# Kernel optimization log

Hardware: AMD Instinct MI355X
Metric: run time of the kernel (lower is better)

Reference implementation:

```python
import jax, jax.numpy as jnp
import numpy as np


def conv2d(x, w, b, pad):
    y = jax.lax.conv_general_dilated(x, w, (1, 1), [(pad, pad), (pad, pad)],
                                     dimension_numbers=('NCHW', 'OIHW', 'NCHW'))
    return y + b[None, :, None, None]


def setup_inputs() -> dict:
    key = jax.random.key(0)
    ks = jax.random.split(key, 24)
    bs, C, OC, K = 2, 64, 3, 3
    hi = wi = 96
    ho = wo = 192

    def _w(k, o, i, kh, kw):
        return jax.random.normal(k, (o, i, kh, kw), jnp.float32) / np.float32(np.sqrt(i * kh * kw))

    inp = {
        'x': jax.random.normal(ks[0], (bs, C, hi, wi), jnp.float32),
        'poseMap': jax.random.normal(ks[1], (1, 3, ho, wo), jnp.float32),
        'interMapY': jax.random.randint(ks[2], (ho, wo), 0, hi, jnp.int32),
        'interMapX': jax.random.randint(ks[3], (ho, wo), 0, wi, jnp.int32),
        # sigmaconv: 3x3 convs 64->64->64->2
        'sig_w1': _w(ks[4], 64, 64, 3, 3), 'sig_b1': jnp.zeros((64,), jnp.float32),
        'sig_w2': _w(ks[5], 64, 64, 3, 3), 'sig_b2': jnp.zeros((64,), jnp.float32),
        'sig_w3': _w(ks[6], 2, 64, 3, 3), 'sig_b3': jnp.zeros((2,), jnp.float32),
        # dwconv: 1x1 convs 3->64->256->C*K*K
        'dw_w1': _w(ks[7], 64, 3, 1, 1), 'dw_b1': jnp.zeros((64,), jnp.float32),
        'dw_w2': _w(ks[8], 256, 64, 1, 1), 'dw_b2': jnp.zeros((256,), jnp.float32),
        'dw_w3': _w(ks[9], C * K * K, 256, 1, 1), 'dw_b3': jnp.zeros((C * K * K,), jnp.float32),
        # pwconv: 1x1 convs 3->64->256->C*OC
        'pw_w1': _w(ks[10], 64, 3, 1, 1), 'pw_b1': jnp.zeros((64,), jnp.float32),
        'pw_w2': _w(ks[11], 256, 64, 1, 1), 'pw_b2': jnp.zeros((256,), jnp.float32),
        'pw_w3': _w(ks[12], C * OC, 256, 1, 1), 'pw_b3': jnp.zeros((C * OC,), jnp.float32),
    }
    return inp


def reference(x, poseMap, interMapY, interMapX,
              sig_w1, sig_b1, sig_w2, sig_b2, sig_w3, sig_b3,
              dw_w1, dw_b1, dw_w2, dw_b2, dw_w3, dw_b3,
              pw_w1, pw_b1, pw_w2, pw_b2, pw_w3, pw_b3):
    C, K, OC = 64, 3, 3
    bs, _, hi, wi = x.shape
    ho, wo = poseMap.shape[2], poseMap.shape[3]
    pad = K // 2

    p = jax.lax.stop_gradient(poseMap)  # original detaches poseMap
    # kernel-predict branches (1x1 conv MLPs over position map)
    dw = conv2d(jax.nn.relu(conv2d(jax.nn.relu(conv2d(p, dw_w1, dw_b1, 0)), dw_w2, dw_b2, 0)), dw_w3, dw_b3, 0)
    dw = dw.reshape(1, C, K * K, ho, wo)
    pw = conv2d(jax.nn.relu(conv2d(jax.nn.relu(conv2d(p, pw_w1, pw_b1, 0)), pw_w2, pw_b2, 0)), pw_w3, pw_b3, 0)
    pw = pw.reshape(C, OC, ho, wo)

    # unfold(x, K, padding=K//2): [bs, C, K*K, hi, wi], kernel taps row-major
    xp = jnp.pad(x, ((0, 0), (0, 0), (pad, pad), (pad, pad)))
    h = jnp.stack([xp[:, :, dy:dy + hi, dx:dx + wi]
                   for dy in range(K) for dx in range(K)], axis=2)
    # irregular spatial gather to HR grid: [bs, C, K*K, ho, wo]
    h = h[:, :, :, interMapY, interMapX]

    mean = jnp.sum(h * jax.nn.softmax(dw, axis=2), axis=2)  # [bs, C, ho, wo]
    sigma = conv2d(jax.nn.relu(conv2d(jax.nn.relu(conv2d(mean, sig_w1, sig_b1, 1)), sig_w2, sig_b2, 1)), sig_w3, sig_b3, 1)
    sigmad = sigma[:, 0:1, None, :, :]
    sigmar = sigma[:, 1:2, None, :, :]
    bw = sigmad * dw + sigmar * jnp.abs(h - mean[:, :, None, :, :])
    xa = jnp.sum(h * jax.nn.softmax(bw, axis=2), axis=2)  # [bs, C, ho, wo]
    out = jnp.einsum('bchw,cohw->bohw', xa, pw)  # [bs, OC, ho, wo]
    return out
```

## Files before the change

kernel.cpp:

```cpp
#include <hip/hip_runtime.h>
#include <hip/hip_bf16.h>

#define NPIX 36864

typedef __attribute__((ext_vector_type(8))) short short8;
typedef __attribute__((ext_vector_type(4))) short short4v;
typedef __attribute__((ext_vector_type(4))) float float4v;

__device__ inline unsigned short f2b(float x) {
    return __builtin_bit_cast(unsigned short, __float2bfloat16(x));
}
__device__ inline float b2f(unsigned short h) {
    return __uint_as_float(((unsigned int)h) << 16);
}

#define WB_TOTAL 312320
#define XCAST_N  1179648
__global__ __launch_bounds__(256) void prep_all(
    const float* __restrict__ dw2, const float* __restrict__ dw3,
    const float* __restrict__ pw2, const float* __restrict__ pw3,
    const float* __restrict__ sw1, const float* __restrict__ sw2,
    const float* __restrict__ sw3, unsigned short* __restrict__ wb,
    const float* __restrict__ x, unsigned short* __restrict__ xb)
{
    int i = blockIdx.x * 256 + threadIdx.x;
    if (i >= WB_TOTAL) {
        int j = i - WB_TOTAL;
        if (j < XCAST_N) xb[j] = f2b(x[j]);
        return;
    }
    unsigned short v;
    if (i < 16384)        v = f2b(dw2[i]);
    else if (i < 32768)   v = f2b(pw2[i - 16384]);
    else if (i < 180224)  v = f2b(dw3[i - 32768]);
    else if (i < 229376)  v = f2b(pw3[i - 180224]);
    else if (i < 266240) { int j = i - 229376; int t = j / 4096, r = j % 4096, oc = r / 64, ic = r % 64;
                           v = f2b(sw1[(oc * 64 + ic) * 9 + t]); }
    else if (i < 303104) { int j = i - 266240; int t = j / 4096, r = j % 4096, oc = r / 64, ic = r % 64;
                           v = f2b(sw2[(oc * 64 + ic) * 9 + t]); }
    else                 { int j = i - 303104; int t = j / 1024, r = j % 1024, oc = r / 64, ic = r % 64;
                           v = (oc < 2) ? f2b(sw3[(oc * 64 + ic) * 9 + t]) : (unsigned short)0; }
    wb[i] = v;
}

__global__ __launch_bounds__(256, 3) void mlp_fused(
    const float* __restrict__ pose,
    const float* __restrict__ w1A, const float* __restrict__ b1A,
    const float* __restrict__ w1B, const float* __restrict__ b1B,
    const unsigned short* __restrict__ w2A, const unsigned short* __restrict__ w2B,
    const float* __restrict__ b2A, const float* __restrict__ b2B,
    const unsigned short* __restrict__ w33,
    const float* __restrict__ b3A, const float* __restrict__ b3B,
    unsigned short* __restrict__ outA, unsigned short* __restrict__ outB)
{
    __shared__ unsigned short sh[16384 + 4096];
    unsigned short* h2s = sh;
    unsigned short* Ts  = sh;
    unsigned short* h1s = sh + 16384;
    const int tid = threadIdx.x;
    const int u = blockIdx.y;
    const int chain = (u == 3) ? 1 : 0;
    const int px0 = blockIdx.x * 64;
    const int w = tid >> 6, l = tid & 63;
    const int ln = l & 15, lkg = l >> 4, lk = lkg * 8;
    const float* w1 = chain ? w1B : w1A;
    const float* b1 = chain ? b1B : b1A;
    const unsigned short* w2 = chain ? w2B : w2A;
    const float* b2 = chain ? b2B : b2A;
    {
        int px = px0 + l;
        float p0 = pose[px], p1 = pose[NPIX + px], p2 = pose[2 * NPIX + px];
        short8 s0, s1;
        #pragma unroll
        for (int j = 0; j < 16; ++j) {
            int oc = w * 16 + j;
            float v = b1[oc] + w1[oc * 3] * p0 + w1[oc * 3 + 1] * p1 + w1[oc * 3 + 2] * p2;
            unsigned short uv = f2b(fmaxf(v, 0.f));
            if (j < 8) s0[j] = (short)uv; else s1[j - 8] = (short)uv;
        }
        *(short8*)&h1s[(w * 2 + 0) * 512 + l * 8] = s0;
        *(short8*)&h1s[(w * 2 + 1) * 512 + l * 8] = s1;
    }
    __syncthreads();
    {
        short8 b0v[4], b1v[4];
        #pragma unroll
        for (int nt = 0; nt < 4; ++nt) {
            b0v[nt] = *(const short8*)&h1s[(lkg    ) * 512 + (nt * 16 + ln) * 8];
            b1v[nt] = *(const short8*)&h1s[(4 + lkg) * 512 + (nt * 16 + ln) * 8];
        }
        float4v acc[4][4] = {};
        #pragma unroll
        for (int mt = 0; mt < 4; ++mt) {
            int ocr = w * 64 + mt * 16 + ln;
            short8 a0 = *(const short8*)&w2[(size_t)ocr * 64 + lk];
            short8 a1 = *(const short8*)&w2[(size_t)ocr * 64 + 32 + lk];
            #pragma unroll
            for (int nt = 0; nt < 4; ++nt) {
                acc[mt][nt] = __builtin_amdgcn_mfma_f32_16x16x32_bf16(a0, b0v[nt], acc[mt][nt], 0, 0, 0);
                acc[mt][nt] = __builtin_amdgcn_mfma_f32_16x16x32_bf16(a1, b1v[nt], acc[mt][nt], 0, 0, 0);
            }
        }
        #pragma unroll
        for (int mt = 0; mt < 4; ++mt) {
            int ocb = w * 64 + mt * 16 + lkg * 4;
            int chk = ocb >> 3, pos = (lkg & 1) * 4;
            float bv0 = b2[ocb + 0], bv1 = b2[ocb + 1], bv2 = b2[ocb + 2], bv3 = b2[ocb + 3];
            #pragma unroll
            for (int nt = 0; nt < 4; ++nt) {
                int pxl = nt * 16 + ln;
                short4v pk;
                pk[0] = (short)f2b(fmaxf(acc[mt][nt][0] + bv0, 0.f));
                pk[1] = (short)f2b(fmaxf(acc[mt][nt][1] + bv1, 0.f));
                pk[2] = (short)f2b(fmaxf(acc[mt][nt][2] + bv2, 0.f));
                pk[3] = (short)f2b(fmaxf(acc[mt][nt][3] + bv3, 0.f));
                *(short4v*)&h2s[chk * 512 + pxl * 8 + pos] = pk;
            }
        }
    }
    __syncthreads();
    const int rowbase = chain ? 576 : u * 192;
    const int obase   = chain ? 0 : u * 192;
    const float* b3 = chain ? b3B : b3A;
    unsigned short* outp = chain ? outB : outA;
    float4v acc[3][4] = {};
    const int r0 = rowbase + w * 48 + ln;
    #pragma unroll
    for (int kc = 0; kc < 8; ++kc) {
        short8 a0 = *(const short8*)&w33[(size_t)(r0 +  0) * 256 + kc * 32 + lk];
        short8 a1 = *(const short8*)&w33[(size_t)(r0 + 16) * 256 + kc * 32 + lk];
        short8 a2 = *(const short8*)&w33[(size_t)(r0 + 32) * 256 + kc * 32 + lk];
        #pragma unroll
        for (int nt = 0; nt < 4; ++nt) {
            short8 b = *(const short8*)&h2s[(kc * 4 + lkg) * 512 + (nt * 16 + ln) * 8];
            acc[0][nt] = __builtin_amdgcn_mfma_f32_16x16x32_bf16(a0, b, acc[0][nt], 0, 0, 0);
            acc[1][nt] = __builtin_amdgcn_mfma_f32_16x16x32_bf16(a1, b, acc[1][nt], 0, 0, 0);
            acc[2][nt] = __builtin_amdgcn_mfma_f32_16x16x32_bf16(a2, b, acc[2][nt], 0, 0, 0);
        }
    }
    __syncthreads();
    #pragma unroll
    for (int mt = 0; mt < 3; ++mt) {
        const int tr = w * 48 + mt * 16 + lkg * 4;
        #pragma unroll
        for (int r = 0; r < 4; ++r) {
            float bv = b3[obase + tr + r];
            #pragma unroll
            for (int nt = 0; nt < 4; ++nt)
                Ts[(tr + r) * 72 + nt * 16 + ln] = f2b(acc[mt][nt][r] + bv);
        }
    }
    __syncthreads();
    for (int i = tid; i < 1536; i += 256) {
        int row = i >> 3, pc = (i & 7) * 8;
        *(short8*)&outp[(size_t)(obase + row) * NPIX + px0 + pc] = *(const short8*)&Ts[row * 72 + pc];
    }
}

template<int MT>
__global__ __launch_bounds__(256) void conv3x3_mfma(
    const unsigned short* __restrict__ act, const unsigned short* __restrict__ wgt,
    const float* __restrict__ bias, unsigned short* __restrict__ out,
    int relu)
{
    constexpr int SP = 72;
    constexpr int OCP = MT * 16;
    __shared__ unsigned short Bs[4 * 66 * SP];
    const int tid = threadIdx.x;
    int bx = blockIdx.x;
    const int xt = bx % 3; bx /= 3;
    const int yg = bx % 96; const int b = bx / 96;
    const int y0 = yg * 2;
    const int x0 = xt * 64;
    const size_t actb = (size_t)b * NPIX * 64;
    const int w = tid >> 6, l = tid & 63;
    const int ln = l & 15, lkg = l >> 4, lk = lkg * 8;
    const int mt = (MT == 4) ? w : 0;
    short8 Wr[9][2];
    #pragma unroll
    for (int t = 0; t < 9; ++t)
        #pragma unroll
        for (int hh = 0; hh < 2; ++hh)
            Wr[t][hh] = *(const short8*)&wgt[((size_t)t * OCP + mt * 16 + ln) * 64 + hh * 32 + lk];
    for (int s = tid; s < 264; s += 256) {
        int r = s / 66, i = s % 66;
        int yy = y0 + r - 1, xx = x0 + i - 1;
        unsigned short* dst = &Bs[(r * 66 + i) * SP];
        if (yy >= 0 && yy < 192 && xx >= 0 && xx < 192) {
            const unsigned short* src = &act[actb + (size_t)(yy * 192 + xx) * 64];
            #pragma unroll
            for (int j = 0; j < 8; ++j) *(short8*)(dst + j * 8) = *(const short8*)(src + j * 8);
        } else {
            short8 z = {};
            #pragma unroll
            for (int j = 0; j < 8; ++j) *(short8*)(dst + j * 8) = z;
        }
    }
    __syncthreads();
    const int NT = (MT == 4) ? 4 : 1;
    const int ntb = (MT == 4) ? 0 : w;
    float4v acc[2][4] = {};
    #pragma unroll
    for (int t = 0; t < 9; ++t) {
        const int r = t / 3, dx = t % 3;
        #pragma unroll
        for (int hh = 0; hh < 2; ++hh) {
            #pragma unroll
            for (int o = 0; o < 2; ++o) {
                #pragma unroll
                for (int n = 0; n < 4; ++n) {
                    if (n >= NT) break;
                    int slot = (o + r) * 66 + (ntb + n) * 16 + ln + dx;
                    short8 bf = *(const short8*)&Bs[slot * SP + hh * 32 + lk];
                    acc[o][n] = __builtin_amdgcn_mfma_f32_16x16x32_bf16(Wr[t][hh], bf, acc[o][n], 0, 0, 0);
                }
            }
        }
    }
    #pragma unroll
    for (int o = 0; o < 2; ++o) {
        #pragma unroll
        for (int n = 0; n < 4; ++n) {
            if (n >= NT) break;
            int px = (y0 + o) * 192 + x0 + (ntb + n) * 16 + ln;
            if (MT == 4) {
                int oc = mt * 16 + lkg * 4;
                float v0 = acc[o][n][0] + bias[oc + 0];
                float v1 = acc[o][n][1] + bias[oc + 1];
                float v2 = acc[o][n][2] + bias[oc + 2];
                float v3 = acc[o][n][3] + bias[oc + 3];
                if (relu) { v0 = fmaxf(v0, 0.f); v1 = fmaxf(v1, 0.f); v2 = fmaxf(v2, 0.f); v3 = fmaxf(v3, 0.f); }
                uint2 pk;
                pk.x = (unsigned int)f2b(v0) | (((unsigned int)f2b(v1)) << 16);
                pk.y = (unsigned int)f2b(v2) | (((unsigned int)f2b(v3)) << 16);
                *(uint2*)&out[((size_t)b * NPIX + px) * 64 + oc] = pk;
            } else if (lkg == 0) {
                float v0 = acc[o][n][0] + bias[0];
                float v1 = acc[o][n][1] + bias[1];
                out[((size_t)b * 2 + 0) * NPIX + px] = f2b(v0);
                out[((size_t)b * 2 + 1) * NPIX + px] = f2b(v1);
            }
        }
    }
}

#define PLSZ 10192
__global__ __launch_bounds__(256) void mean_k(
    const unsigned short* __restrict__ xb, const int* __restrict__ imy, const int* __restrict__ imx,
    const unsigned short* __restrict__ dw, unsigned short* __restrict__ mean_cm)
{
    __shared__ unsigned short pl[PLSZ];
    const int c = blockIdx.y;
    const int px0 = blockIdx.x * 1024;
    const int tid = threadIdx.x;
    {
        short8 z = {};
        short8* pf = (short8*)pl;
        for (int i = tid; i < PLSZ / 8; i += 256) pf[i] = z;
    }
    float wk[4][9];
    int base[4];
    #pragma unroll
    for (int q = 0; q < 4; ++q) {
        int px = px0 + q * 256 + tid;
        base[q] = imy[px] * 104 + imx[px] + 3;
        float d[9];
        #pragma unroll
        for (int k = 0; k < 9; ++k) d[k] = b2f(dw[(size_t)(c * 9 + k) * NPIX + px]);
        float m = d[0];
        #pragma unroll
        for (int k = 1; k < 9; ++k) m = fmaxf(m, d[k]);
        float s = 0.f;
        #pragma unroll
        for (int k = 0; k < 9; ++k) { wk[q][k] = __expf(d[k] - m); s += wk[q][k]; }
        float inv = 1.f / s;
        #pragma unroll
        for (int k = 0; k < 9; ++k) wk[q][k] *= inv;
    }
    #pragma unroll
    for (int b = 0; b < 2; ++b) {
        __syncthreads();
        const unsigned short* xp = xb + (size_t)(b * 64 + c) * 9216;
        for (int i = tid; i < 96 * 12; i += 256) {
            int row = i / 12, ch = i % 12;
            const short4v* src = (const short4v*)&xp[row * 96 + ch * 8];
            unsigned short* dd = &pl[(row + 1) * 104 + 4 + ch * 8];
            *(short4v*)dd = src[0];
            *(short4v*)(dd + 4) = src[1];
        }
        __syncthreads();
        #pragma unroll
        for (int q = 0; q < 4; ++q) {
            int px = px0 + q * 256 + tid;
            float a = 0.f;
            #pragma unroll
            for (int k = 0; k < 9; ++k)
                a += wk[q][k] * b2f(pl[base[q] + (k / 3) * 104 + (k % 3)]);
            mean_cm[(size_t)(b * 64 + c) * NPIX + px] = f2b(a);
        }
    }
}

__global__ __launch_bounds__(256) void tr_k(
    const unsigned short* __restrict__ in, unsigned short* __restrict__ out)
{
    __shared__ unsigned short T[64 * 68];
    int px0 = blockIdx.x * 64;
    int b = blockIdx.y;
    int tid = threadIdx.x;
    for (int i = tid; i < 4096; i += 256) {
        int c = i >> 6, p = i & 63;
        T[p * 68 + c] = in[(size_t)(b * 64 + c) * NPIX + px0 + p];
    }
    __syncthreads();
    for (int i = tid; i < 4096; i += 256) {
        int p = i >> 6, c = i & 63;
        out[((size_t)b * NPIX + px0 + p) * 64 + c] = T[p * 68 + c];
    }
}

__global__ __launch_bounds__(256) void xa_k(
    const unsigned short* __restrict__ xb, const int* __restrict__ imy, const int* __restrict__ imx,
    const unsigned short* __restrict__ dw, const unsigned short* __restrict__ mean_cm,
    const unsigned short* __restrict__ sigma, unsigned short* __restrict__ xab)
{
    __shared__ unsigned short pl[PLSZ];
    const int c = blockIdx.y;
    const int px0 = blockIdx.x * 1024;
    const int tid = threadIdx.x;
    {
        short8 z = {};
        short8* pf = (short8*)pl;
        for (int i = tid; i < PLSZ / 8; i += 256) pf[i] = z;
    }
    float d[4][9];
    int base[4];
    #pragma unroll
    for (int q = 0; q < 4; ++q) {
        int px = px0 + q * 256 + tid;
        base[q] = imy[px] * 104 + imx[px] + 3;
        #pragma unroll
        for (int k = 0; k < 9; ++k) d[q][k] = b2f(dw[(size_t)(c * 9 + k) * NPIX + px]);
    }
    #pragma unroll
    for (int b = 0; b < 2; ++b) {
        __syncthreads();
        const unsigned short* xp = xb + (size_t)(b * 64 + c) * 9216;
        for (int i = tid; i < 96 * 12; i += 256) {
            int row = i / 12, ch = i % 12;
            const short4v* src = (const short4v*)&xp[row * 96 + ch * 8];
            unsigned short* dd = &pl[(row + 1) * 104 + 4 + ch * 8];
            *(short4v*)dd = src[0];
            *(short4v*)(dd + 4) = src[1];
        }
        __syncthreads();
        #pragma unroll
        for (int q = 0; q < 4; ++q) {
            int px = px0 + q * 256 + tid;
            float mn = b2f(mean_cm[(size_t)(b * 64 + c) * NPIX + px]);
            float sd = b2f(sigma[((size_t)b * 2 + 0) * NPIX + px]);
            float sr = b2f(sigma[((size_t)b * 2 + 1) * NPIX + px]);
            float h[9], bw[9];
            #pragma unroll
            for (int k = 0; k < 9; ++k) {
                h[k] = b2f(pl[base[q] + (k / 3) * 104 + (k % 3)]);
                bw[k] = sd * d[q][k] + sr * fabsf(h[k] - mn);
            }
            float m = bw[0];
            #pragma unroll
            for (int k = 1; k < 9; ++k) m = fmaxf(m, bw[k]);
            float s = 0.f, a = 0.f;
            #pragma unroll
            for (int k = 0; k < 9; ++k) { float e = __expf(bw[k] - m); s += e; a += e * h[k]; }
            xab[(size_t)(b * 64 + c) * NPIX + px] = f2b(a / s);
        }
    }
}

__global__ __launch_bounds__(256) void einsum_k(
    const unsigned short* __restrict__ xab, const unsigned short* __restrict__ pw,
    float* __restrict__ out)
{
    __shared__ float red[3][4][64];
    const int tid = threadIdx.x;
    const int pxl = tid & 63, cq = tid >> 6;
    const int px = blockIdx.x * 64 + pxl;
    const int b = blockIdx.y;
    float a0 = 0.f, a1 = 0.f, a2 = 0.f;
    #pragma unroll
    for (int ci = 0; ci < 16; ++ci) {
        int c = cq * 16 + ci;
        float v = b2f(xab[(size_t)(b * 64 + c) * NPIX + px]);
        a0 += v * b2f(pw[(size_t)(c * 3 + 0) * NPIX + px]);
        a1 += v * b2f(pw[(size_t)(c * 3 + 1) * NPIX + px]);
        a2 += v * b2f(pw[(size_t)(c * 3 + 2) * NPIX + px]);
    }
    red[0][cq][pxl] = a0;
    red[1][cq][pxl] = a1;
    red[2][cq][pxl] = a2;
    __syncthreads();
    if (cq < 3) {
        float s = red[cq][0][pxl] + red[cq][1][pxl] + red[cq][2][pxl] + red[cq][3][pxl];
        out[((size_t)b * 3 + cq) * NPIX + px] = s;
    }
}

extern "C" void kernel_launch(void* const* d_in, const int* in_sizes, int n_in,
                              void* d_out, int out_size, void* d_ws, size_t ws_size,
                              hipStream_t stream)
{
    (void)in_sizes; (void)n_in; (void)out_size; (void)ws_size;
    const float* x      = (const float*)d_in[0];
    const float* pose   = (const float*)d_in[1];
    const int*   imy    = (const int*)d_in[2];
    const int*   imx    = (const int*)d_in[3];
    const float* sig_w1 = (const float*)d_in[4];
    const float* sig_b1 = (const float*)d_in[5];
    const float* sig_w2 = (const float*)d_in[6];
    const float* sig_b2 = (const float*)d_in[7];
    const float* sig_w3 = (const float*)d_in[8];
    const float* sig_b3 = (const float*)d_in[9];
    const float* dw_w1  = (const float*)d_in[10];
    const float* dw_b1  = (const float*)d_in[11];
    const float* dw_w2  = (const float*)d_in[12];
    const float* dw_b2  = (const float*)d_in[13];
    const float* dw_w3  = (const float*)d_in[14];
    const float* dw_b3  = (const float*)d_in[15];
    const float* pw_w1  = (const float*)d_in[16];
    const float* pw_b1  = (const float*)d_in[17];
    const float* pw_w2  = (const float*)d_in[18];
    const float* pw_b2  = (const float*)d_in[19];
    const float* pw_w3  = (const float*)d_in[20];
    const float* pw_b3  = (const float*)d_in[21];
    float* out = (float*)d_out;

    unsigned short* ws = (unsigned short*)d_ws;
    size_t off = 0;
    unsigned short* wb      = ws + off; off += WB_TOTAL;
    unsigned short* xb16    = ws + off; off += (size_t)XCAST_N;
    unsigned short* dwbuf   = ws + off; off += (size_t)576 * NPIX;
    unsigned short* pwbuf   = ws + off; off += (size_t)192 * NPIX;
    unsigned short* mean_cm = ws + off; off += (size_t)2 * 64 * NPIX;
    unsigned short* mean_pm = ws + off; off += (size_t)2 * NPIX * 64;
    unsigned short* s1      = ws + off; off += (size_t)2 * NPIX * 64;
    unsigned short* s2      = ws + off; off += (size_t)2 * NPIX * 64;
    unsigned short* sigma   = ws + off; off += (size_t)2 * 2 * NPIX;
    unsigned short* xab     = ws + off; off += (size_t)2 * 64 * NPIX;

    unsigned short* w_dw2 = wb + 0;
    unsigned short* w_pw2 = wb + 16384;
    unsigned short* w_33  = wb + 32768;
    unsigned short* w_s1t = wb + 229376;
    unsigned short* w_s2t = wb + 266240;
    unsigned short* w_s3t = wb + 303104;

    dim3 blk(256);
    prep_all<<<dim3((WB_TOTAL + XCAST_N + 255) / 256), blk, 0, stream>>>(
        dw_w2, dw_w3, pw_w2, pw_w3, sig_w1, sig_w2, sig_w3, wb, x, xb16);
    mlp_fused<<<dim3(576, 4), blk, 0, stream>>>(
        pose, dw_w1, dw_b1, pw_w1, pw_b1, w_dw2, w_pw2, dw_b2, pw_b2,
        w_33, dw_b3, pw_b3, dwbuf, pwbuf);
    mean_k<<<dim3(36, 64), blk, 0, stream>>>(xb16, imy, imx, dwbuf, mean_cm);
    tr_k<<<dim3(576, 2), blk, 0, stream>>>(mean_cm, mean_pm);
    conv3x3_mfma<4><<<dim3(576), blk, 0, stream>>>(mean_pm, w_s1t, sig_b1, s1, 1);
    conv3x3_mfma<4><<<dim3(576), blk, 0, stream>>>(s1,      w_s2t, sig_b2, s2, 1);
    conv3x3_mfma<1><<<dim3(576), blk, 0, stream>>>(s2,      w_s3t, sig_b3, sigma, 0);
    xa_k<<<dim3(36, 64), blk, 0, stream>>>(xb16, imy, imx, dwbuf, mean_cm, sigma, xab);
    einsum_k<<<dim3(576, 2), blk, 0, stream>>>(xab, pwbuf, out);
}
```

Baseline: 248.7 us.

## Stage layer-3 weights into swizzled LDS with double-buffered async loads

The final 1x1 layer of the fused MLP kernel now loads its weight tile into LDS in four K-quarters using async global_load_lds. The loads are double-buffered and XOR-swizzled so each quarter's fetch overlaps the MFMA work on the previous quarter, replacing direct per-lane global loads inside the MFMA loop. Shared memory grows from about 40KB to about 80KB and the occupancy hint drops from 3 to 2 blocks per CU, trading occupancy for hidden weight-load latency. The extra barriers between quarters also add synchronisation cost.

```diff
diff --git a/kernel.cpp b/kernel.cpp
--- a/kernel.cpp
+++ b/kernel.cpp
@@ -43,7 +43,7 @@
     wb[i] = v;
 }
 
-__global__ __launch_bounds__(256, 3) void mlp_fused(
+__global__ __launch_bounds__(256, 2) void mlp_fused(
     const float* __restrict__ pose,
     const float* __restrict__ w1A, const float* __restrict__ b1A,
     const float* __restrict__ w1B, const float* __restrict__ b1B,
@@ -53,10 +53,12 @@
     const float* __restrict__ b3A, const float* __restrict__ b3B,
     unsigned short* __restrict__ outA, unsigned short* __restrict__ outB)
 {
-    __shared__ unsigned short sh[16384 + 4096];
+    __shared__ unsigned short sh[16384 + 12288 + 12288];
     unsigned short* h2s = sh;
     unsigned short* Ts  = sh;
-    unsigned short* h1s = sh + 16384;
+    unsigned short* WqA = sh + 16384;
+    unsigned short* WqB = sh + 16384 + 12288;
+    unsigned short* h1s = WqB;
     const int tid = threadIdx.x;
     const int u = blockIdx.y;
     const int chain = (u == 3) ? 1 : 0;
@@ -67,6 +69,46 @@
     const float* b1 = chain ? b1B : b1A;
     const unsigned short* w2 = chain ? w2B : w2A;
     const float* b2 = chain ? b2B : b2A;
+    const int rowbase = chain ? 576 : u * 192;
+    const int obase   = chain ? 0 : u * 192;
+    const float* b3 = chain ? b3B : b3A;
+    unsigned short* outp = chain ? outB : outA;
+
+    auto stage_wq = [&](int q, unsigned short* buf) {
+        #pragma unroll
+        for (int i = 0; i < 6; ++i) {
+            const int chunk = (i * 4 + w) * 1024;
+            int a  = chunk + l * 16;
+            int ap = a ^ (((a >> 7) & 7) << 4);
+            const unsigned short* gp =
+                &w33[(size_t)(rowbase + (ap >> 7)) * 256 + q * 64 + ((ap & 127) >> 1)];
+            __builtin_amdgcn_global_load_lds(
+                (const __attribute__((address_space(1))) void*)gp,
+                (__attribute__((address_space(3))) void*)((char*)buf + chunk),
+                16, 0, 0);
+        }
+    };
+    float4v acc[3][4] = {};
+    auto l3_quarter = [&](int q, const unsigned short* buf) {
+        #pragma unroll
+        for (int kl = 0; kl < 2; ++kl) {
+            const int kc = q * 2 + kl;
+            const int r0 = w * 48 + ln;
+            const int sw = (r0 & 7) << 4;
+            short8 a0 = *(const short8*)((const char*)buf + (((r0     ) * 128 + kl * 64 + lkg * 16) ^ sw));
+            short8 a1 = *(const short8*)((const char*)buf + (((r0 + 16) * 128 + kl * 64 + lkg * 16) ^ sw));
+            short8 a2 = *(const short8*)((const char*)buf + (((r0 + 32) * 128 + kl * 64 + lkg * 16) ^ sw));
+            #pragma unroll
+            for (int nt = 0; nt < 4; ++nt) {
+                short8 b = *(const short8*)&h2s[(kc * 4 + lkg) * 512 + (nt * 16 + ln) * 8];
+                acc[0][nt] = __builtin_amdgcn_mfma_f32_16x16x32_bf16(a0, b, acc[0][nt], 0, 0, 0);
+                acc[1][nt] = __builtin_amdgcn_mfma_f32_16x16x32_bf16(a1, b, acc[1][nt], 0, 0, 0);
+                acc[2][nt] = __builtin_amdgcn_mfma_f32_16x16x32_bf16(a2, b, acc[2][nt], 0, 0, 0);
+            }
+        }
+    };
+
+    stage_wq(0, WqA);
     {
         int px = px0 + l;
         float p0 = pose[px], p1 = pose[NPIX + px], p2 = pose[2 * NPIX + px];
@@ -89,7 +131,7 @@
             b0v[nt] = *(const short8*)&h1s[(lkg    ) * 512 + (nt * 16 + ln) * 8];
             b1v[nt] = *(const short8*)&h1s[(4 + lkg) * 512 + (nt * 16 + ln) * 8];
         }
-        float4v acc[4][4] = {};
+        float4v acc2[4][4] = {};
         #pragma unroll
         for (int mt = 0; mt < 4; ++mt) {
             int ocr = w * 64 + mt * 16 + ln;
@@ -97,8 +139,8 @@
             short8 a1 = *(const short8*)&w2[(size_t)ocr * 64 + 32 + lk];
             #pragma unroll
             for (int nt = 0; nt < 4; ++nt) {
-                acc[mt][nt] = __builtin_amdgcn_mfma_f32_16x16x32_bf16(a0, b0v[nt], acc[mt][nt], 0, 0, 0);
-                acc[mt][nt] = __builtin_amdgcn_mfma_f32_16x16x32_bf16(a1, b1v[nt], acc[mt][nt], 0, 0, 0);
+                acc2[mt][nt] = __builtin_amdgcn_mfma_f32_16x16x32_bf16(a0, b0v[nt], acc2[mt][nt], 0, 0, 0);
+                acc2[mt][nt] = __builtin_amdgcn_mfma_f32_16x16x32_bf16(a1, b1v[nt], acc2[mt][nt], 0, 0, 0);
             }
         }
         #pragma unroll
@@ -110,34 +152,25 @@
             for (int nt = 0; nt < 4; ++nt) {
                 int pxl = nt * 16 + ln;
                 short4v pk;
-                pk[0] = (short)f2b(fmaxf(acc[mt][nt][0] + bv0, 0.f));
-                pk[1] = (short)f2b(fmaxf(acc[mt][nt][1] + bv1, 0.f));
-                pk[2] = (short)f2b(fmaxf(acc[mt][nt][2] + bv2, 0.f));
-                pk[3] = (short)f2b(fmaxf(acc[mt][nt][3] + bv3, 0.f));
+                pk[0] = (short)f2b(fmaxf(acc2[mt][nt][0] + bv0, 0.f));
+                pk[1] = (short)f2b(fmaxf(acc2[mt][nt][1] + bv1, 0.f));
+                pk[2] = (short)f2b(fmaxf(acc2[mt][nt][2] + bv2, 0.f));
+                pk[3] = (short)f2b(fmaxf(acc2[mt][nt][3] + bv3, 0.f));
                 *(short4v*)&h2s[chk * 512 + pxl * 8 + pos] = pk;
             }
         }
     }
     __syncthreads();
-    const int rowbase = chain ? 576 : u * 192;
-    const int obase   = chain ? 0 : u * 192;
-    const float* b3 = chain ? b3B : b3A;
-    unsigned short* outp = chain ? outB : outA;
-    float4v acc[3][4] = {};
-    const int r0 = rowbase + w * 48 + ln;
-    #pragma unroll
-    for (int kc = 0; kc < 8; ++kc) {
-        short8 a0 = *(const short8*)&w33[(size_t)(r0 +  0) * 256 + kc * 32 + lk];
-        short8 a1 = *(const short8*)&w33[(size_t)(r0 + 16) * 256 + kc * 32 + lk];
-        short8 a2 = *(const short8*)&w33[(size_t)(r0 + 32) * 256 + kc * 32 + lk];
-        #pragma unroll
-        for (int nt = 0; nt < 4; ++nt) {
-            short8 b = *(const short8*)&h2s[(kc * 4 + lkg) * 512 + (nt * 16 + ln) * 8];
-            acc[0][nt] = __builtin_amdgcn_mfma_f32_16x16x32_bf16(a0, b, acc[0][nt], 0, 0, 0);
-            acc[1][nt] = __builtin_amdgcn_mfma_f32_16x16x32_bf16(a1, b, acc[1][nt], 0, 0, 0);
-            acc[2][nt] = __builtin_amdgcn_mfma_f32_16x16x32_bf16(a2, b, acc[2][nt], 0, 0, 0);
-        }
-    }
+    stage_wq(1, WqB);
+    l3_quarter(0, WqA);
+    __syncthreads();
+    stage_wq(2, WqA);
+    l3_quarter(1, WqB);
+    __syncthreads();
+    stage_wq(3, WqB);
+    l3_quarter(2, WqA);
+    __syncthreads();
+    l3_quarter(3, WqB);
     __syncthreads();
     #pragma unroll
     for (int mt = 0; mt < 3; ++mt) {
```

After: 238.9 us. -3.9%, faster.

## Make mlp_fused persistent over pixel tiles with LDS-resident swizzled layer-3 weights

Applied to the files above, without the earlier changes.

The MLP kernel now launches 64x4 blocks, each looping over 9 tiles of 64 pixels. The 192x256 layer-3 weight slice is loaded once into 96KB of LDS via global_load_lds with an XOR swizzle. Layer-2 weights stay in registers, and the next tile's pose values are prefetched. This removes the per-tile global reloads of weights, at the cost of one block per CU, only 256 blocks, and extra barriers per iteration.

```diff
diff --git a/kernel.cpp b/kernel.cpp
--- a/kernel.cpp
+++ b/kernel.cpp
@@ -43,7 +43,7 @@
     wb[i] = v;
 }
 
-__global__ __launch_bounds__(256, 3) void mlp_fused(
+__global__ __launch_bounds__(256, 1) void mlp_fused(
     const float* __restrict__ pose,
     const float* __restrict__ w1A, const float* __restrict__ b1A,
     const float* __restrict__ w1B, const float* __restrict__ b1B,
@@ -53,107 +53,139 @@
     const float* __restrict__ b3A, const float* __restrict__ b3B,
     unsigned short* __restrict__ outA, unsigned short* __restrict__ outB)
 {
-    __shared__ unsigned short sh[16384 + 4096];
-    unsigned short* h2s = sh;
-    unsigned short* Ts  = sh;
-    unsigned short* h1s = sh + 16384;
+    __shared__ unsigned short sh[65536];
+    unsigned short* Ws  = sh;
+    unsigned short* h2s = sh + 49152;
+    unsigned short* h1s = h2s;
+    unsigned short* Ts  = h2s;
     const int tid = threadIdx.x;
     const int u = blockIdx.y;
     const int chain = (u == 3) ? 1 : 0;
-    const int px0 = blockIdx.x * 64;
     const int w = tid >> 6, l = tid & 63;
     const int ln = l & 15, lkg = l >> 4, lk = lkg * 8;
     const float* w1 = chain ? w1B : w1A;
     const float* b1 = chain ? b1B : b1A;
     const unsigned short* w2 = chain ? w2B : w2A;
     const float* b2 = chain ? b2B : b2A;
-    {
-        int px = px0 + l;
-        float p0 = pose[px], p1 = pose[NPIX + px], p2 = pose[2 * NPIX + px];
-        short8 s0, s1;
-        #pragma unroll
-        for (int j = 0; j < 16; ++j) {
-            int oc = w * 16 + j;
-            float v = b1[oc] + w1[oc * 3] * p0 + w1[oc * 3 + 1] * p1 + w1[oc * 3 + 2] * p2;
-            unsigned short uv = f2b(fmaxf(v, 0.f));
-            if (j < 8) s0[j] = (short)uv; else s1[j - 8] = (short)uv;
-        }
-        *(short8*)&h1s[(w * 2 + 0) * 512 + l * 8] = s0;
-        *(short8*)&h1s[(w * 2 + 1) * 512 + l * 8] = s1;
-    }
-    __syncthreads();
-    {
-        short8 b0v[4], b1v[4];
-        #pragma unroll
-        for (int nt = 0; nt < 4; ++nt) {
-            b0v[nt] = *(const short8*)&h1s[(lkg    ) * 512 + (nt * 16 + ln) * 8];
-            b1v[nt] = *(const short8*)&h1s[(4 + lkg) * 512 + (nt * 16 + ln) * 8];
-        }
-        float4v acc[4][4] = {};
-        #pragma unroll
-        for (int mt = 0; mt < 4; ++mt) {
-            int ocr = w * 64 + mt * 16 + ln;
-            short8 a0 = *(const short8*)&w2[(size_t)ocr * 64 + lk];
-            short8 a1 = *(const short8*)&w2[(size_t)ocr * 64 + 32 + lk];
-            #pragma unroll
-            for (int nt = 0; nt < 4; ++nt) {
-                acc[mt][nt] = __builtin_amdgcn_mfma_f32_16x16x32_bf16(a0, b0v[nt], acc[mt][nt], 0, 0, 0);
-                acc[mt][nt] = __builtin_amdgcn_mfma_f32_16x16x32_bf16(a1, b1v[nt], acc[mt][nt], 0, 0, 0);
-            }
-        }
-        #pragma unroll
-        for (int mt = 0; mt < 4; ++mt) {
-            int ocb = w * 64 + mt * 16 + lkg * 4;
-            int chk = ocb >> 3, pos = (lkg & 1) * 4;
-            float bv0 = b2[ocb + 0], bv1 = b2[ocb + 1], bv2 = b2[ocb + 2], bv3 = b2[ocb + 3];
-            #pragma unroll
-            for (int nt = 0; nt < 4; ++nt) {
-                int pxl = nt * 16 + ln;
-                short4v pk;
-                pk[0] = (short)f2b(fmaxf(acc[mt][nt][0] + bv0, 0.f));
-                pk[1] = (short)f2b(fmaxf(acc[mt][nt][1] + bv1, 0.f));
-                pk[2] = (short)f2b(fmaxf(acc[mt][nt][2] + bv2, 0.f));
-                pk[3] = (short)f2b(fmaxf(acc[mt][nt][3] + bv3, 0.f));
-                *(short4v*)&h2s[chk * 512 + pxl * 8 + pos] = pk;
-            }
-        }
-    }
-    __syncthreads();
     const int rowbase = chain ? 576 : u * 192;
     const int obase   = chain ? 0 : u * 192;
     const float* b3 = chain ? b3B : b3A;
     unsigned short* outp = chain ? outB : outA;
-    float4v acc[3][4] = {};
-    const int r0 = rowbase + w * 48 + ln;
-    #pragma unroll
-    for (int kc = 0; kc < 8; ++kc) {
-        short8 a0 = *(const short8*)&w33[(size_t)(r0 +  0) * 256 + kc * 32 + lk];
-        short8 a1 = *(const short8*)&w33[(size_t)(r0 + 16) * 256 + kc * 32 + lk];
-        short8 a2 = *(const short8*)&w33[(size_t)(r0 + 32) * 256 + kc * 32 + lk];
+
+    for (int i = 0; i < 24; ++i) {
+        const int chunk = (i * 4 + w) * 1024;
+        int a  = chunk + l * 16;
+        int ap = a ^ (((a >> 9) & 7) << 4);
+        const unsigned short* gp =
+            &w33[(size_t)(rowbase + (ap >> 9)) * 256 + ((ap & 511) >> 1)];
+        __builtin_amdgcn_global_load_lds(
+            (const __attribute__((address_space(1))) void*)gp,
+            (__attribute__((address_space(3))) void*)((char*)Ws + chunk),
+            16, 0, 0);
+    }
+    short8 Aw2[4][2];
+    #pragma unroll
+    for (int mt = 0; mt < 4; ++mt) {
+        int ocr = w * 64 + mt * 16 + ln;
+        Aw2[mt][0] = *(const short8*)&w2[(size_t)ocr * 64 + lk];
+        Aw2[mt][1] = *(const short8*)&w2[(size_t)ocr * 64 + 32 + lk];
+    }
+    const int pxbase = blockIdx.x * 576;
+    float p0 = pose[pxbase + l], p1 = pose[NPIX + pxbase + l], p2 = pose[2 * NPIX + pxbase + l];
+
+    for (int it = 0; it < 9; ++it) {
+        const int px0 = pxbase + it * 64;
+        {
+            short8 s0, s1;
+            #pragma unroll
+            for (int j = 0; j < 16; ++j) {
+                int oc = w * 16 + j;
+                float v = b1[oc] + w1[oc * 3] * p0 + w1[oc * 3 + 1] * p1 + w1[oc * 3 + 2] * p2;
+                unsigned short uv = f2b(fmaxf(v, 0.f));
+                if (j < 8) s0[j] = (short)uv; else s1[j - 8] = (short)uv;
+            }
+            *(short8*)&h1s[(w * 2 + 0) * 512 + l * 8] = s0;
+            *(short8*)&h1s[(w * 2 + 1) * 512 + l * 8] = s1;
+        }
+        float np0 = 0.f, np1 = 0.f, np2 = 0.f;
+        if (it < 8) {
+            int pxn = px0 + 64 + l;
+            np0 = pose[pxn]; np1 = pose[NPIX + pxn]; np2 = pose[2 * NPIX + pxn];
+        }
+        __syncthreads();
+        short8 b0v[4], b1v[4];
         #pragma unroll
         for (int nt = 0; nt < 4; ++nt) {
-            short8 b = *(const short8*)&h2s[(kc * 4 + lkg) * 512 + (nt * 16 + ln) * 8];
-            acc[0][nt] = __builtin_amdgcn_mfma_f32_16x16x32_bf16(a0, b, acc[0][nt], 0, 0, 0);
-            acc[1][nt] = __builtin_amdgcn_mfma_f32_16x16x32_bf16(a1, b, acc[1][nt], 0, 0, 0);
-            acc[2][nt] = __builtin_amdgcn_mfma_f32_16x16x32_bf16(a2, b, acc[2][nt], 0, 0, 0);
-        }
-    }
-    __syncthreads();
-    #pragma unroll
-    for (int mt = 0; mt < 3; ++mt) {
-        const int tr = w * 48 + mt * 16 + lkg * 4;
-        #pragma unroll
-        for (int r = 0; r < 4; ++r) {
-            float bv = b3[obase + tr + r];
-            #pragma unroll
-            for (int nt = 0; nt < 4; ++nt)
-                Ts[(tr + r) * 72 + nt * 16 + ln] = f2b(acc[mt][nt][r] + bv);
-        }
-    }
-    __syncthreads();
-    for (int i = tid; i < 1536; i += 256) {
-        int row = i >> 3, pc = (i & 7) * 8;
-        *(short8*)&outp[(size_t)(obase + row) * NPIX + px0 + pc] = *(const short8*)&Ts[row * 72 + pc];
+            b0v[nt] = *(const short8*)&h1s[(lkg    ) * 512 + (nt * 16 + ln) * 8];
+            b1v[nt] = *(const short8*)&h1s[(4 + lkg) * 512 + (nt * 16 + ln) * 8];
+        }
+        __syncthreads();
+        {
+            float4v acc2[4][4] = {};
+            #pragma unroll
+            for (int mt = 0; mt < 4; ++mt) {
+                #pragma unroll
+                for (int nt = 0; nt < 4; ++nt) {
+                    acc2[mt][nt] = __builtin_amdgcn_mfma_f32_16x16x32_bf16(Aw2[mt][0], b0v[nt], acc2[mt][nt], 0, 0, 0);
+                    acc2[mt][nt] = __builtin_amdgcn_mfma_f32_16x16x32_bf16(Aw2[mt][1], b1v[nt], acc2[mt][nt], 0, 0, 0);
+                }
+            }
+            #pragma unroll
+            for (int mt = 0; mt < 4; ++mt) {
+                int ocb = w * 64 + mt * 16 + lkg * 4;
+                int chk = ocb >> 3, pos = (lkg & 1) * 4;
+                float bv0 = b2[ocb + 0], bv1 = b2[ocb + 1], bv2 = b2[ocb + 2], bv3 = b2[ocb + 3];
+                #pragma unroll
+                for (int nt = 0; nt < 4; ++nt) {
+                    int pxl = nt * 16 + ln;
+                    short4v pk;
+                    pk[0] = (short)f2b(fmaxf(acc2[mt][nt][0] + bv0, 0.f));
+                    pk[1] = (short)f2b(fmaxf(acc2[mt][nt][1] + bv1, 0.f));
+                    pk[2] = (short)f2b(fmaxf(acc2[mt][nt][2] + bv2, 0.f));
+                    pk[3] = (short)f2b(fmaxf(acc2[mt][nt][3] + bv3, 0.f));
+                    *(short4v*)&h2s[chk * 512 + pxl * 8 + pos] = pk;
+                }
+            }
+        }
+        __syncthreads();
+        float4v acc[3][4] = {};
+        {
+            const int r0l = w * 48 + ln;
+            const int swz = (r0l & 7) << 4;
+            const char* Wb = (const char*)Ws;
+            #pragma unroll
+            for (int kc = 0; kc < 8; ++kc) {
+                short8 a0 = *(const short8*)(Wb + (((r0l     ) * 512 + kc * 64 + lk * 2) ^ swz));
+                short8 a1 = *(const short8*)(Wb + (((r0l + 16) * 512 + kc * 64 + lk * 2) ^ swz));
+                short8 a2 = *(const short8*)(Wb + (((r0l + 32) * 512 + kc * 64 + lk * 2) ^ swz));
+                #pragma unroll
+                for (int nt = 0; nt < 4; ++nt) {
+                    short8 b = *(const short8*)&h2s[(kc * 4 + lkg) * 512 + (nt * 16 + ln) * 8];
+                    acc[0][nt] = __builtin_amdgcn_mfma_f32_16x16x32_bf16(a0, b, acc[0][nt], 0, 0, 0);
+                    acc[1][nt] = __builtin_amdgcn_mfma_f32_16x16x32_bf16(a1, b, acc[1][nt], 0, 0, 0);
+                    acc[2][nt] = __builtin_amdgcn_mfma_f32_16x16x32_bf16(a2, b, acc[2][nt], 0, 0, 0);
+                }
+            }
+        }
+        __syncthreads();
+        #pragma unroll
+        for (int mt = 0; mt < 3; ++mt) {
+            const int tr = w * 48 + mt * 16 + lkg * 4;
+            #pragma unroll
+            for (int r = 0; r < 4; ++r) {
+                float bv = b3[obase + tr + r];
+                #pragma unroll
+                for (int nt = 0; nt < 4; ++nt)
+                    Ts[(tr + r) * 72 + nt * 16 + ln] = f2b(acc[mt][nt][r] + bv);
+            }
+        }
+        __syncthreads();
+        for (int i = tid; i < 1536; i += 256) {
+            int row = i >> 3, pc = (i & 7) * 8;
+            *(short8*)&outp[(size_t)(obase + row) * NPIX + px0 + pc] = *(const short8*)&Ts[row * 72 + pc];
+        }
+        __syncthreads();
+        p0 = np0; p1 = np1; p2 = np2;
     }
 }
 
@@ -457,7 +489,7 @@
     dim3 blk(256);
     prep_all<<<dim3((WB_TOTAL + XCAST_N + 255) / 256), blk, 0, stream>>>(
         dw_w2, dw_w3, pw_w2, pw_w3, sig_w1, sig_w2, sig_w3, wb, x, xb16);
-    mlp_fused<<<dim3(576, 4), blk, 0, stream>>>(
+    mlp_fused<<<dim3(64, 4), blk, 0, stream>>>(
         pose, dw_w1, dw_b1, pw_w1, pw_b1, w_dw2, w_pw2, dw_b2, pw_b2,
         w_33, dw_b3, pw_b3, dwbuf, pwbuf);
     mean_k<<<dim3(36, 64), blk, 0, stream>>>(xb16, imy, imx, dwbuf, mean_cm);
```

Result: faster. 234.8 us (-5.6%).
